# Kernel tuning notes

Measured on AMD Instinct MI355X. Metric: run time of the kernel, lower is better.

Reference implementation:

```python
import jax, jax.numpy as jnp
import numpy as np

BETA = 0.9       # snn.Leaky beta
THR = 1.0        # snn.Leaky default threshold
NUM_STEPS = 25
P_DROP = 0.2


def setup_inputs() -> dict:
    key = jax.random.key(0)
    k0, k1, k2, k3, k4 = jax.random.split(key, 5)
    B, D_IN, D_H, D_OUT = 4096, 512, 1024, 256
    x = jax.random.normal(k0, (B, D_IN), dtype=jnp.float32)
    # nn.Linear-style init: U(-1/sqrt(fan_in), 1/sqrt(fan_in))
    s1 = 1.0 / np.sqrt(D_IN)
    s2 = 1.0 / np.sqrt(D_H)
    w1 = jax.random.uniform(k1, (D_H, D_IN), jnp.float32, -s1, s1)
    b1 = jax.random.uniform(k2, (D_H,), jnp.float32, -s1, s1)
    w2 = jax.random.uniform(k3, (D_OUT, D_H), jnp.float32, -s2, s2)
    b2 = jax.random.uniform(k4, (D_OUT,), jnp.float32, -s2, s2)
    return {"x": x, "w1": w1, "b1": b1, "w2": w2, "b2": b2}


def reference(x, w1, b1, w2, b2):
    dt = x.dtype
    heav = lambda u: (u > 0).astype(dt)
    # cur1 = fc1(x) is identical every step (x is constant) -> hoist out of loop
    cur1 = x @ w1.T + b1                      # [B, D_H]
    B = x.shape[0]
    mem1_0 = jnp.zeros((B, w1.shape[0]), dt)
    mem2_0 = jnp.zeros((B, w2.shape[0]), dt)
    drop_keys = jax.random.split(jax.random.key(42), NUM_STEPS)

    def step(carry, k):
        mem1, mem2 = carry
        # Leaky (reset_mechanism='subtract'): reset from previous mem (detached)
        r1 = heav(mem1 - THR)
        mem1 = BETA * mem1 + cur1 - r1 * THR
        spk1 = heav(mem1 - THR)
        # training-mode Dropout(p=0.2)
        mask = jax.random.bernoulli(k, 1.0 - P_DROP, spk1.shape)
        spk1d = jnp.where(mask, spk1 / (1.0 - P_DROP), jnp.zeros((), dt))
        cur2 = spk1d @ w2.T + b2              # [B, D_OUT]
        r2 = heav(mem2 - THR)
        mem2 = BETA * mem2 + cur2 - r2 * THR
        spk2 = heav(mem2 - THR)
        return (mem1, mem2), (jax.nn.sigmoid(spk2), jax.nn.sigmoid(mem2))

    _, (spk2_rec, mem2_rec) = jax.lax.scan(step, (mem1_0, mem2_0), drop_keys)
    return spk2_rec, mem2_rec                 # each [NUM_STEPS, B, D_OUT]
```

## Files before the change

kernel.cpp:

```cpp
#include <hip/hip_runtime.h>
#include <stdint.h>

#define T_STEPS 25
#define BB   4096
#define DIN  512
#define DH   1024
#define DOUT 256

typedef float f32x2 __attribute__((ext_vector_type(2)));

struct Keys { uint32_t a[T_STEPS]; uint32_t b[T_STEPS]; };

__host__ __device__ __forceinline__ void tf2x32(uint32_t k0, uint32_t k1,
                                                uint32_t x0, uint32_t x1,
                                                uint32_t& y0, uint32_t& y1) {
  const uint32_t ks2 = k0 ^ k1 ^ 0x1BD11BDAu;
  x0 += k0; x1 += k1;
#define TFR(r) { x0 += x1; x1 = (x1 << (r)) | (x1 >> (32 - (r))); x1 ^= x0; }
  TFR(13) TFR(15) TFR(26) TFR(6)   x0 += k1;  x1 += ks2 + 1u;
  TFR(17) TFR(29) TFR(16) TFR(24)  x0 += ks2; x1 += k0 + 2u;
  TFR(13) TFR(15) TFR(26) TFR(6)   x0 += k0;  x1 += k1 + 3u;
  TFR(17) TFR(29) TFR(16) TFR(24)  x0 += k1;  x1 += ks2 + 4u;
  TFR(13) TFR(15) TFR(26) TFR(6)   x0 += ks2; x1 += k0 + 5u;
#undef TFR
  y0 = x0; y1 = x1;
}

__device__ __forceinline__ bool keep_f(uint32_t ka, uint32_t kb, uint32_t e) {
  uint32_t y0, y1;
  tf2x32(ka, kb, 0u, e, y0, y1);
  return (((y0 ^ y1) >> 9) <= 6710886u);
}

__global__ __launch_bounds__(256) void k_trt(const float* __restrict__ in,
                                             float* __restrict__ out, int H, int K) {
  __shared__ float tile[32][33];
  const int bh = blockIdx.x * 32, bk = blockIdx.y * 32;
  const int tx = threadIdx.x & 31, ty = threadIdx.x >> 5;
#pragma unroll
  for (int r = ty; r < 32; r += 8)
    tile[r][tx] = in[(size_t)(bh + r) * K + bk + tx];
  __syncthreads();
#pragma unroll
  for (int r = ty; r < 32; r += 8)
    out[(size_t)(bk + r) * H + bh + tx] = tile[tx][r];
}

__global__ __launch_bounds__(256) void k_cur1s(const float* __restrict__ xT,
                                               const float* __restrict__ w1t,
                                               const float* __restrict__ b1,
                                               float* __restrict__ cur1) {
  const int b  = blockIdx.x * 256 + threadIdx.x;
  const int h0 = blockIdx.y * 32;
  f32x2 acc2[16];
#pragma unroll
  for (int i = 0; i < 16; ++i) acc2[i] = (f32x2){0.f, 0.f};
  for (int k = 0; k < DIN; ++k) {
    float xv = xT[(size_t)k * BB + b];
    f32x2 xv2 = {xv, xv};
    const f32x2* wk2 = (const f32x2*)(w1t + (size_t)k * DH + h0);
#pragma unroll
    for (int q = 0; q < 16; ++q) {
      f32x2 wv = wk2[q];
      asm("v_pk_fma_f32 %0, %2, %1, %0" : "+v"(acc2[q]) : "v"(xv2), "s"(wv));
    }
  }
  float* dst = cur1 + (size_t)b * DH + h0;
#pragma unroll
  for (int i = 0; i < 16; ++i) {
    float2 v;
    v.x = __fadd_rn(acc2[i].x, b1[h0 + i*2 + 0]);
    v.y = __fadd_rn(acc2[i].y, b1[h0 + i*2 + 1]);
    *(float2*)(dst + i*2) = v;
  }
}

__global__ __launch_bounds__(256) void k_trajf(const float* __restrict__ cur1,
                                               uint32_t* __restrict__ maskT, Keys kk) {
  const int e = blockIdx.x * 256 + threadIdx.x;
  const int lane = threadIdx.x & 63;
  const int b = e >> 10;
  const int w = (e >> 5) & 31;
  const float c = cur1[e];
  float m = 0.0f;
  for (int t = 0; t < T_STEPS; ++t) {
    float r = (m > 1.0f) ? 1.0f : 0.0f;
    m = __fsub_rn(__fadd_rn(__fmul_rn(0.9f, m), c), r);
    bool spk = m > 1.0f;
    bool kp = keep_f(kk.a[t], kk.b[t], (uint32_t)e);
    unsigned long long ball = __ballot(spk && kp);
    if ((lane & 31) == 0)
      maskT[((size_t)t * 32 + w) * BB + b] = (uint32_t)(ball >> (lane & 32));
  }
}

__global__ __launch_bounds__(256) void k_gemm2(const uint32_t* __restrict__ maskT,
                                               const float* __restrict__ w2t,
                                               float* __restrict__ cur2) {
  const int row = blockIdx.x * 256 + threadIdx.x;
  const int t = row >> 12, b = row & 4095;
  const int o0 = blockIdx.y * 32;
  const uint32_t* mrow = maskT + (size_t)t * 32 * BB + b;
  f32x2 acc2[16];
#pragma unroll
  for (int i = 0; i < 16; ++i) acc2[i] = (f32x2){0.f, 0.f};
  for (int w = 0; w < 32; ++w) {
    const uint32_t word = mrow[(size_t)w * BB];
    const float* wp = w2t + (size_t)(w * 32) * DOUT + o0;
#pragma unroll 2
    for (int j = 0; j < 32; ++j) {
      int bm = ((int)(word << (31 - j))) >> 31;
      float sel = __int_as_float(bm & 0x3FA00000);
      f32x2 sel2 = {sel, sel};
      const f32x2* wk2 = (const f32x2*)(wp + (size_t)j * DOUT);
#pragma unroll
      for (int q = 0; q < 16; ++q) {
        f32x2 wv = wk2[q];
        asm("v_pk_fma_f32 %0, %2, %1, %0" : "+v"(acc2[q]) : "v"(sel2), "s"(wv));
      }
    }
  }
  float* dst = cur2 + (size_t)row * DOUT + o0;
#pragma unroll
  for (int q = 0; q < 4; ++q) {
    float4 v0 = make_float4(acc2[q*4+0].x, acc2[q*4+0].y, acc2[q*4+1].x, acc2[q*4+1].y);
    float4 v1 = make_float4(acc2[q*4+2].x, acc2[q*4+2].y, acc2[q*4+3].x, acc2[q*4+3].y);
    *(float4*)(dst + q*8)     = v0;
    *(float4*)(dst + q*8 + 4) = v1;
  }
}

__global__ __launch_bounds__(256) void k_out2(const float* __restrict__ b2,
                                              float* __restrict__ out) {
  const int b = blockIdx.x;
  const int o = threadIdx.x;
  float* out1 = out + (size_t)T_STEPS * BB * DOUT;
  const float bb = b2[o];
  float m = 0.0f;
  for (int t = 0; t < T_STEPS; ++t) {
    size_t p = ((size_t)t * BB + b) * DOUT + o;
    float c2 = __fadd_rn(out1[p], bb);
    float r = (m > 1.0f) ? 1.0f : 0.0f;
    m = __fsub_rn(__fadd_rn(__fmul_rn(0.9f, m), c2), r);
    out[p]  = (m > 1.0f) ? 0.7310585786300049f : 0.5f;
    out1[p] = 1.0f / (1.0f + __expf(-m));
  }
}

extern "C" void kernel_launch(void* const* d_in, const int* in_sizes, int n_in,
                              void* d_out, int out_size, void* d_ws, size_t ws_size,
                              hipStream_t stream) {
  const float* x  = (const float*)d_in[0];
  const float* w1 = (const float*)d_in[1];
  const float* b1 = (const float*)d_in[2];
  const float* w2 = (const float*)d_in[3];
  const float* b2 = (const float*)d_in[4];
  float* out = (float*)d_out;
  char* ws = (char*)d_ws;

  float*    w1t   = (float*)(ws);
  float*    w2t   = (float*)(ws + 2097152);
  float*    xT    = (float*)(ws + 3145728);
  float*    cur1  = (float*)(ws + 11534336);
  uint32_t* maskT = (uint32_t*)(ws + 28311552);
  float*    cur2  = out + (size_t)T_STEPS * BB * DOUT;

  Keys kk;
  for (int t = 0; t < T_STEPS; ++t) {
    uint32_t y0, y1;
    tf2x32(0u, 42u, 0u, (uint32_t)t, y0, y1);
    kk.a[t] = y0; kk.b[t] = y1;
  }

  k_trt<<<dim3(DH / 32, DIN / 32), 256, 0, stream>>>(w1, w1t, DH, DIN);
  k_trt<<<dim3(DOUT / 32, DH / 32), 256, 0, stream>>>(w2, w2t, DOUT, DH);
  k_trt<<<dim3(BB / 32, DIN / 32), 256, 0, stream>>>(x, xT, BB, DIN);
  k_cur1s<<<dim3(BB / 256, DH / 32), 256, 0, stream>>>(xT, w1t, b1, cur1);
  k_trajf<<<dim3(BB * DH / 256), 256, 0, stream>>>(cur1, maskT, kk);
  k_gemm2<<<dim3(T_STEPS * BB / 256, DOUT / 32), 256, 0, stream>>>(maskT, w2t, cur2);
  k_out2<<<dim3(BB), 256, 0, stream>>>(b2, out);
}
```

Baseline: 928.7 us.

## Process two batch rows per thread in gemm2 with packed FMA op_sel

Each thread in the second GEMM now computes two batch rows (b and b+2048) at once. The two rows' mask bits are packed into one f32x2 selector, and op_sel broadcasts each scalar weight across the pair. This halves the grid and the number of weight loads per output and raises per-thread work, at the cost of doubling the accumulator registers. A launch-bounds occupancy hint is added.

```diff
diff --git a/kernel.cpp b/kernel.cpp
--- a/kernel.cpp
+++ b/kernel.cpp
@@ -94,39 +94,47 @@
   }
 }
 
-__global__ __launch_bounds__(256) void k_gemm2(const uint32_t* __restrict__ maskT,
-                                               const float* __restrict__ w2t,
-                                               float* __restrict__ cur2) {
-  const int row = blockIdx.x * 256 + threadIdx.x;
-  const int t = row >> 12, b = row & 4095;
+__global__ __launch_bounds__(256, 4) void k_gemm2(const uint32_t* __restrict__ maskT,
+                                                  const float* __restrict__ w2t,
+                                                  float* __restrict__ cur2) {
+  const int t  = blockIdx.x >> 3;
+  const int b  = ((blockIdx.x & 7) << 8) + threadIdx.x;
   const int o0 = blockIdx.y * 32;
   const uint32_t* mrow = maskT + (size_t)t * 32 * BB + b;
-  f32x2 acc2[16];
+  f32x2 accp[32];
 #pragma unroll
-  for (int i = 0; i < 16; ++i) acc2[i] = (f32x2){0.f, 0.f};
+  for (int i = 0; i < 32; ++i) accp[i] = (f32x2){0.f, 0.f};
   for (int w = 0; w < 32; ++w) {
-    const uint32_t word = mrow[(size_t)w * BB];
+    const uint32_t wordA = mrow[(size_t)w * BB];
+    const uint32_t wordB = mrow[(size_t)w * BB + 2048];
     const float* wp = w2t + (size_t)(w * 32) * DOUT + o0;
 #pragma unroll 2
     for (int j = 0; j < 32; ++j) {
-      int bm = ((int)(word << (31 - j))) >> 31;
-      float sel = __int_as_float(bm & 0x3FA00000);
-      f32x2 sel2 = {sel, sel};
+      int bmA = ((int)(wordA << (31 - j))) >> 31;
+      int bmB = ((int)(wordB << (31 - j))) >> 31;
+      f32x2 sel2;
+      sel2.x = __int_as_float(bmA & 0x3FA00000);
+      sel2.y = __int_as_float(bmB & 0x3FA00000);
       const f32x2* wk2 = (const f32x2*)(wp + (size_t)j * DOUT);
 #pragma unroll
       for (int q = 0; q < 16; ++q) {
         f32x2 wv = wk2[q];
-        asm("v_pk_fma_f32 %0, %2, %1, %0" : "+v"(acc2[q]) : "v"(sel2), "s"(wv));
+        asm("v_pk_fma_f32 %0, %1, %2, %0 op_sel:[0,0,0] op_sel_hi:[1,0,1]"
+            : "+v"(accp[2*q]) : "v"(sel2), "s"(wv));
+        asm("v_pk_fma_f32 %0, %1, %2, %0 op_sel:[0,1,0] op_sel_hi:[1,1,1]"
+            : "+v"(accp[2*q+1]) : "v"(sel2), "s"(wv));
       }
     }
   }
-  float* dst = cur2 + (size_t)row * DOUT + o0;
+  const size_t rowA = (size_t)t * BB + b;
+  float* dstA = cur2 + rowA * DOUT + o0;
+  float* dstB = cur2 + (rowA + 2048) * DOUT + o0;
 #pragma unroll
-  for (int q = 0; q < 4; ++q) {
-    float4 v0 = make_float4(acc2[q*4+0].x, acc2[q*4+0].y, acc2[q*4+1].x, acc2[q*4+1].y);
-    float4 v1 = make_float4(acc2[q*4+2].x, acc2[q*4+2].y, acc2[q*4+3].x, acc2[q*4+3].y);
-    *(float4*)(dst + q*8)     = v0;
-    *(float4*)(dst + q*8 + 4) = v1;
+  for (int q = 0; q < 8; ++q) {
+    float4 vA = make_float4(accp[q*4+0].x, accp[q*4+1].x, accp[q*4+2].x, accp[q*4+3].x);
+    float4 vB = make_float4(accp[q*4+0].y, accp[q*4+1].y, accp[q*4+2].y, accp[q*4+3].y);
+    *(float4*)(dstA + q*4) = vA;
+    *(float4*)(dstB + q*4) = vB;
   }
 }
 
@@ -177,6 +185,6 @@
   k_trt<<<dim3(BB / 32, DIN / 32), 256, 0, stream>>>(x, xT, BB, DIN);
   k_cur1s<<<dim3(BB / 256, DH / 32), 256, 0, stream>>>(xT, w1t, b1, cur1);
   k_trajf<<<dim3(BB * DH / 256), 256, 0, stream>>>(cur1, maskT, kk);
-  k_gemm2<<<dim3(T_STEPS * BB / 256, DOUT / 32), 256, 0, stream>>>(maskT, w2t, cur2);
+  k_gemm2<<<dim3(T_STEPS * 8, DOUT / 32), 256, 0, stream>>>(maskT, w2t, cur2);
   k_out2<<<dim3(BB), 256, 0, stream>>>(b2, out);
 }
```

Result: slower. 1.011 ms (+8.8%).

## Fuse fc1 GEMM with spike-trajectory mask generation; prefetch mask words in gemm2

Applied to the files above, without the earlier changes.

Merges the cur1 GEMM kernel with the leaky-neuron trajectory and dropout mask kernel. Each thread keeps its 32 cur1 values in registers and builds each packed mask word itself, where before a wave ballot was used. This removes the 16 MB cur1 write and read round trip and one launch. The cost is higher register pressure, serial Threefry hashing per thread (32 elements x 25 steps), and a fused kernel with only 512 blocks. It also prefetches the next mask word in gemm2 to hide load latency.

```diff
diff --git a/kernel.cpp b/kernel.cpp
--- a/kernel.cpp
+++ b/kernel.cpp
@@ -46,10 +46,10 @@
     out[(size_t)(bk + r) * H + bh + tx] = tile[tx][r];
 }
 
-__global__ __launch_bounds__(256) void k_cur1s(const float* __restrict__ xT,
+__global__ __launch_bounds__(256) void k_fused(const float* __restrict__ xT,
                                                const float* __restrict__ w1t,
                                                const float* __restrict__ b1,
-                                               float* __restrict__ cur1) {
+                                               uint32_t* __restrict__ maskT, Keys kk) {
   const int b  = blockIdx.x * 256 + threadIdx.x;
   const int h0 = blockIdx.y * 32;
   f32x2 acc2[16];
@@ -65,32 +65,27 @@
       asm("v_pk_fma_f32 %0, %2, %1, %0" : "+v"(acc2[q]) : "v"(xv2), "s"(wv));
     }
   }
-  float* dst = cur1 + (size_t)b * DH + h0;
+  float cur[32], m[32];
 #pragma unroll
   for (int i = 0; i < 16; ++i) {
-    float2 v;
-    v.x = __fadd_rn(acc2[i].x, b1[h0 + i*2 + 0]);
-    v.y = __fadd_rn(acc2[i].y, b1[h0 + i*2 + 1]);
-    *(float2*)(dst + i*2) = v;
+    cur[i*2+0] = __fadd_rn(acc2[i].x, b1[h0 + i*2 + 0]);
+    cur[i*2+1] = __fadd_rn(acc2[i].y, b1[h0 + i*2 + 1]);
+    m[i*2+0] = 0.0f; m[i*2+1] = 0.0f;
   }
-}
-
-__global__ __launch_bounds__(256) void k_trajf(const float* __restrict__ cur1,
-                                               uint32_t* __restrict__ maskT, Keys kk) {
-  const int e = blockIdx.x * 256 + threadIdx.x;
-  const int lane = threadIdx.x & 63;
-  const int b = e >> 10;
-  const int w = (e >> 5) & 31;
-  const float c = cur1[e];
-  float m = 0.0f;
+  const uint32_t e0 = (uint32_t)(b * DH + h0);
+  uint32_t* mdst = maskT + (size_t)(h0 >> 5) * BB + b;
   for (int t = 0; t < T_STEPS; ++t) {
-    float r = (m > 1.0f) ? 1.0f : 0.0f;
-    m = __fsub_rn(__fadd_rn(__fmul_rn(0.9f, m), c), r);
-    bool spk = m > 1.0f;
-    bool kp = keep_f(kk.a[t], kk.b[t], (uint32_t)e);
-    unsigned long long ball = __ballot(spk && kp);
-    if ((lane & 31) == 0)
-      maskT[((size_t)t * 32 + w) * BB + b] = (uint32_t)(ball >> (lane & 32));
+    uint32_t word = 0;
+    const uint32_t ka = kk.a[t], kb = kk.b[t];
+#pragma unroll
+    for (int i = 0; i < 32; ++i) {
+      float r = (m[i] > 1.0f) ? 1.0f : 0.0f;
+      m[i] = __fsub_rn(__fadd_rn(__fmul_rn(0.9f, m[i]), cur[i]), r);
+      bool spk = m[i] > 1.0f;
+      bool kp = keep_f(ka, kb, e0 + i);
+      word |= (uint32_t)(spk && kp) << i;
+    }
+    mdst[(size_t)t * 32 * BB] = word;
   }
 }
 
@@ -104,8 +99,9 @@
   f32x2 acc2[16];
 #pragma unroll
   for (int i = 0; i < 16; ++i) acc2[i] = (f32x2){0.f, 0.f};
+  uint32_t word = mrow[0];
   for (int w = 0; w < 32; ++w) {
-    const uint32_t word = mrow[(size_t)w * BB];
+    const uint32_t wnext = (w < 31) ? mrow[(size_t)(w + 1) * BB] : 0u;
     const float* wp = w2t + (size_t)(w * 32) * DOUT + o0;
 #pragma unroll 2
     for (int j = 0; j < 32; ++j) {
@@ -119,6 +115,7 @@
         asm("v_pk_fma_f32 %0, %2, %1, %0" : "+v"(acc2[q]) : "v"(sel2), "s"(wv));
       }
     }
+    word = wnext;
   }
   float* dst = cur2 + (size_t)row * DOUT + o0;
 #pragma unroll
@@ -161,8 +158,7 @@
   float*    w1t   = (float*)(ws);
   float*    w2t   = (float*)(ws + 2097152);
   float*    xT    = (float*)(ws + 3145728);
-  float*    cur1  = (float*)(ws + 11534336);
-  uint32_t* maskT = (uint32_t*)(ws + 28311552);
+  uint32_t* maskT = (uint32_t*)(ws + 11534336);
   float*    cur2  = out + (size_t)T_STEPS * BB * DOUT;
 
   Keys kk;
@@ -175,8 +171,7 @@
   k_trt<<<dim3(DH / 32, DIN / 32), 256, 0, stream>>>(w1, w1t, DH, DIN);
   k_trt<<<dim3(DOUT / 32, DH / 32), 256, 0, stream>>>(w2, w2t, DOUT, DH);
   k_trt<<<dim3(BB / 32, DIN / 32), 256, 0, stream>>>(x, xT, BB, DIN);
-  k_cur1s<<<dim3(BB / 256, DH / 32), 256, 0, stream>>>(xT, w1t, b1, cur1);
-  k_trajf<<<dim3(BB * DH / 256), 256, 0, stream>>>(cur1, maskT, kk);
+  k_fused<<<dim3(BB / 256, DH / 32), 256, 0, stream>>>(xT, w1t, b1, maskT, kk);
   k_gemm2<<<dim3(T_STEPS * BB / 256, DOUT / 32), 256, 0, stream>>>(maskT, w2t, cur2);
   k_out2<<<dim3(BB), 256, 0, stream>>>(b2, out);
 }
```

After: 912.0 us. Within noise of the previous version (-1.8%).
